# Kernel tuning notes

Hardware: AMD Instinct MI355X
Metric: run time of the kernel (lower is better)

Reference implementation:

```python
import jax, jax.numpy as jnp
import numpy as np

IMG_W, IMG_H = 704, 256
BN_EPS, LN_EPS = 1e-5, 1e-5


def _l2norm(x, axis):
    n = jnp.linalg.norm(x, axis=axis, keepdims=True)
    return x / jnp.maximum(n, 1e-12)


def _layernorm(x, g, b):
    m = jnp.mean(x, axis=-1, keepdims=True)
    v = jnp.var(x, axis=-1, keepdims=True)
    return (x - m) / jnp.sqrt(v + LN_EPS) * g + b


def _bilinear(ref, uv):
    # ref: (B, d, H, W); uv: (B, P, 2) pixel coords (x, y)
    B, d, H, W = ref.shape
    x, y = uv[..., 0], uv[..., 1]
    x0 = jnp.floor(x); y0 = jnp.floor(y)
    wx = x - x0; wy = y - y0
    valid = (x >= 0) & (x <= W - 1) & (y >= 0) & (y <= H - 1)
    x0i = jnp.clip(x0.astype(jnp.int32), 0, W - 1)
    x1i = jnp.clip(x0i + 1, 0, W - 1)
    y0i = jnp.clip(y0.astype(jnp.int32), 0, H - 1)
    y1i = jnp.clip(y0i + 1, 0, H - 1)
    ref_t = ref.reshape(B, d, H * W).transpose(0, 2, 1)  # (B, HW, d)
    g = lambda yy, xx: jnp.take_along_axis(ref_t, (yy * W + xx)[..., None], axis=1)
    val = (g(y0i, x0i) * ((1 - wx) * (1 - wy))[..., None]
           + g(y0i, x1i) * (wx * (1 - wy))[..., None]
           + g(y1i, x0i) * ((1 - wx) * wy)[..., None]
           + g(y1i, x1i) * (wx * wy)[..., None])  # (B, P, d)
    return val, valid.astype(ref.dtype)


def setup_inputs() -> dict:
    key = jax.random.key(0)
    ks = jax.random.split(key, 12)
    b, n, fd, dim, h, w = 2, 6, 128, 128, 64, 176
    feature = jax.random.normal(ks[0], (b, n, fd, h, w), jnp.float32)
    # intrinsics ~ [[500,0,352],[0,500,128],[0,0,1]]
    K = jnp.array([[500.0, 0.0, IMG_W / 2], [0.0, 500.0, IMG_H / 2], [0.0, 0.0, 1.0]], jnp.float32)
    I_src = jnp.broadcast_to(K, (b, n, 3, 3)).copy()
    I_tar_inv = jnp.broadcast_to(jnp.linalg.inv(K), (b, 3, 3)).copy()
    # extrinsics near identity: small rotation + small translation
    a = 0.02 * jax.random.normal(ks[1], (b, n, 3), jnp.float32)
    zeros = jnp.zeros((b, n), jnp.float32)
    skew = jnp.stack([
        jnp.stack([zeros, -a[..., 2], a[..., 1]], -1),
        jnp.stack([a[..., 2], zeros, -a[..., 0]], -1),
        jnp.stack([-a[..., 1], a[..., 0], zeros], -1)], -2)
    R = jnp.eye(3, dtype=jnp.float32) + skew
    T = 0.1 * jax.random.normal(ks[2], (b, n, 3, 1), jnp.float32)
    E = jnp.broadcast_to(jnp.eye(4, dtype=jnp.float32), (b, n, 4, 4)).copy()
    E = E.at[..., :3, :3].set(R).at[..., :3, 3:4].set(T)
    dis = 1.5 * jnp.ones((b, 1, 1, 1), jnp.float32)
    norm = jnp.array([0.0, 0.0, 1.0], jnp.float32)[None, None] + 0.01 * jax.random.normal(ks[3], (b, 1, 3), jnp.float32)
    s = 1.0 / np.sqrt(fd)
    return {
        'feature': feature, 'I_src': I_src, 'I_tar_inv': I_tar_inv, 'E': E, 'dis': dis, 'norm': norm,
        'conv_w': s * jax.random.normal(ks[4], (dim, fd), jnp.float32),
        'bn_gamma': jnp.ones((fd,), jnp.float32), 'bn_beta': jnp.zeros((fd,), jnp.float32),
        'bn_mean': 0.1 * jax.random.normal(ks[5], (fd,), jnp.float32),
        'bn_var': jax.random.uniform(ks[6], (fd,), jnp.float32, 0.5, 1.5),
        'ln1_g': jnp.ones((dim,), jnp.float32), 'ln1_b': jnp.zeros((dim,), jnp.float32),
        'ln2_g': jnp.ones((dim,), jnp.float32), 'ln2_b': jnp.zeros((dim,), jnp.float32),
        'mlp_w1': s * jax.random.normal(ks[7], (dim, 2 * dim), jnp.float32),
        'mlp_b1': jnp.zeros((2 * dim,), jnp.float32),
        'mlp_w2': (1.0 / np.sqrt(2 * fd)) * jax.random.normal(ks[8], (2 * dim, dim), jnp.float32),
        'mlp_b2': jnp.zeros((dim,), jnp.float32),
    }


def reference(feature, I_src, I_tar_inv, E, dis, norm, conv_w, bn_gamma, bn_beta, bn_mean, bn_var,
              ln1_g, ln1_b, ln2_g, ln2_b, mlp_w1, mlp_b1, mlp_w2, mlp_b2):
    b, n, fd, h, w = feature.shape
    dim = conv_w.shape[0]
    P = h * w
    # ---- pixel grid in [0,1], homogeneous ----
    xs = jnp.linspace(0.0, 1.0, w, dtype=feature.dtype)
    ys = jnp.linspace(0.0, 1.0, h, dtype=feature.dtype)
    X, Y = jnp.meshgrid(xs, ys)  # (h, w), x varies along width
    pix = jnp.stack([X, Y, jnp.ones_like(X)], 0).reshape(3, P)  # (3, P)
    img_wh1 = jnp.array([[IMG_W], [IMG_H], [1.0]], feature.dtype)  # (3,1)
    pix = pix * img_wh1
    # ---- homography H = I_src (R - T n^T / dis) I_tar_inv ----
    R = E[..., :3, :3]
    T = E[..., :3, 3:4]
    Hm = I_src @ (R - (T @ norm[:, None, :, :]) / dis) @ I_tar_inv[:, None, :, :]  # (b,n,3,3)
    homo = jnp.einsum('bnij,jp->bnip', Hm, pix)  # (b,n,3,P)
    homo = homo[:, :, :2] / homo[:, :, 2:]
    homo = homo / img_wh1[:2]  # back to 0..1
    uv = homo.transpose(0, 1, 3, 2).reshape(b * n, P, 2) * jnp.array([w, h], feature.dtype)
    # ---- feature_linear: BN(eval) -> ReLU -> 1x1 conv ----
    xf = (feature - bn_mean[:, None, None]) / jnp.sqrt(bn_var + BN_EPS)[:, None, None]
    xf = xf * bn_gamma[:, None, None] + bn_beta[:, None, None]
    xf = jax.nn.relu(xf)
    val = jnp.einsum('oc,bnchw->bnohw', conv_w, xf)  # (b,n,dim,h,w)
    query = val[:, 0]  # (b,dim,h,w)
    # ---- homography-guided bilinear sampling ----
    v, mask = _bilinear(val.reshape(b * n, dim, h, w), uv)  # (bn,P,dim), (bn,P)
    key_n = _l2norm(v, axis=2).reshape(b, n, P, dim)
    q = _l2norm(query.reshape(b, dim, P), axis=1)
    dot = jnp.einsum('bdp,bnpd->bnp', q, key_n)
    dot = dot * mask.reshape(b, n, P)
    att = jax.nn.softmax(dot, axis=1)
    z = jnp.einsum('bnp,bnpd->bpd', att, v.reshape(b, n, P, dim))
    z = z.transpose(0, 2, 1).reshape(b, dim, h, w)
    z = query + z
    # ---- MLP block ----
    z = z.reshape(b, dim, P).transpose(0, 2, 1)  # (b,P,dim)
    z = _layernorm(z, ln1_g, ln1_b)
    hdn = jax.nn.gelu(z @ mlp_w1 + mlp_b1, approximate=False)
    z = z + (hdn @ mlp_w2 + mlp_b2)
    z = _layernorm(z, ln2_g, ln2_b)
    return z.transpose(0, 2, 1).reshape(b, dim, h, w)
```

## Files before the change

### kernel.cpp

```cpp
#include <hip/hip_runtime.h>
#include <hip/hip_bf16.h>
#include <cstdint>
#include <cstddef>

#define B_   2
#define N_   6
#define FD_  128
#define DIM_ 128
#define H_   64
#define W_   176
#define P_   (H_*W_)
#define IMGW 704.0
#define IMGH 256.0
#define UVB  8

struct __align__(16) Samp { float wx, wy; int o00, o01; int o10, o11; int valid, pad; };

typedef __attribute__((ext_vector_type(8))) short short8;
typedef __attribute__((ext_vector_type(4))) float f32x4;

__device__ __forceinline__ float wave_sum(float v) {
#pragma unroll
  for (int off = 32; off > 0; off >>= 1) v += __shfl_xor(v, off, 64);
  return v;
}

__device__ __forceinline__ unsigned short f2bf(float f) {
  union { __hip_bfloat16 h; unsigned short u; } c;
  c.h = __float2bfloat16(f);
  return c.u;
}
__device__ __forceinline__ float bf2f(unsigned short s) {
  return __uint_as_float(((unsigned int)s) << 16);
}
__device__ __forceinline__ float bfx(uint2 u, int j) {
  unsigned int w = (j < 2) ? u.x : u.y;
  return bf2f((unsigned short)((j & 1) ? (w >> 16) : (w & 0xffffu)));
}

__global__ __launch_bounds__(256) void prep_kernel(const float* __restrict__ I_src, const float* __restrict__ I_tar_inv,
                           const float* __restrict__ E, const float* __restrict__ dis,
                           const float* __restrict__ nrm,
                           const float* __restrict__ bn_g, const float* __restrict__ bn_b,
                           const float* __restrict__ bn_m, const float* __restrict__ bn_v,
                           const float* __restrict__ w1, const float* __restrict__ w2,
                           const float* __restrict__ conv_w,
                           Samp* __restrict__ samp, float* __restrict__ bns, float* __restrict__ bnb,
                           short* __restrict__ w1b, short* __restrict__ w2b, short* __restrict__ cwb) {
  int blk = blockIdx.x;
  if (blk >= B_ * N_ * UVB) {
    int tid = (blk - B_ * N_ * UVB) * 256 + threadIdx.x;
    int f = tid >> 6, l = tid & 63;
    if (f < 64) {
      int nt = f >> 2, ks = f & 3;
      int n = nt * 16 + (l & 15);
      int kb = ks * 32 + (l >> 4) * 8;
#pragma unroll
      for (int j = 0; j < 8; ++j)
        w1b[((size_t)f * 64 + l) * 8 + j] = (short)f2bf(w1[(size_t)(kb + j) * 256 + n]);
    } else if (f < 128) {
      int g = f - 64;
      int nt = g >> 3, ks = g & 7;
      int n = nt * 16 + (l & 15);
      int kb = ks * 32 + (l >> 4) * 8;
#pragma unroll
      for (int j = 0; j < 8; ++j)
        w2b[((size_t)g * 64 + l) * 8 + j] = (short)f2bf(w2[(size_t)(kb + j) * 128 + n]);
    } else {
      int g2 = f - 128;
      int ot = g2 >> 2, ks = g2 & 3;
      int o  = ot * 16 + (l & 15);
      int cb = ks * 32 + (l >> 4) * 8;
#pragma unroll
      for (int j = 0; j < 8; ++j)
        cwb[((size_t)g2 * 64 + l) * 8 + j] = (short)f2bf(conv_w[(size_t)o * FD_ + cb + j]);
    }
    return;
  }
  int bn = blk / UVB;
  int part = blk % UVB;
  int bb = bn / N_;
  if (blk == 0 && threadIdx.x < FD_) {
    int t = threadIdx.x;
    float inv = 1.0f / sqrtf(bn_v[t] + 1e-5f);
    float sc = bn_g[t] * inv;
    bns[t] = sc;
    bnb[t] = bn_b[t] - bn_m[t] * sc;
  }
  const float* Ep = E + bn * 16;
  double R[9], T[3];
#pragma unroll
  for (int i = 0; i < 3; ++i) {
#pragma unroll
    for (int j = 0; j < 3; ++j) R[i*3+j] = (double)Ep[i*4+j];
    T[i] = (double)Ep[i*4+3];
  }
  double dd = (double)dis[bb];
  double M[9];
#pragma unroll
  for (int i = 0; i < 3; ++i)
#pragma unroll
    for (int j = 0; j < 3; ++j)
      M[i*3+j] = R[i*3+j] - T[i] * (double)nrm[bb*3+j] / dd;
  const float* Is = I_src + bn * 9;
  double A[9];
#pragma unroll
  for (int i = 0; i < 3; ++i)
#pragma unroll
    for (int j = 0; j < 3; ++j)
      A[i*3+j] = (double)Is[i*3+0]*M[0+j] + (double)Is[i*3+1]*M[3+j] + (double)Is[i*3+2]*M[6+j];
  const float* It = I_tar_inv + bb * 9;
  double Hm[9];
#pragma unroll
  for (int i = 0; i < 3; ++i)
#pragma unroll
    for (int j = 0; j < 3; ++j)
      Hm[i*3+j] = A[i*3+0]*(double)It[0+j] + A[i*3+1]*(double)It[3+j] + A[i*3+2]*(double)It[6+j];

  const double dx = 1.0 / (double)(W_ - 1);
  const double dy = 1.0 / (double)(H_ - 1);
  for (int p = part * 256 + threadIdx.x; p < P_; p += 256 * UVB) {
    int ii = p / W_;
    int jj = p - ii * W_;
    double xs = (jj == W_ - 1) ? 1.0 : (double)jj * dx;
    double ys = (ii == H_ - 1) ? 1.0 : (double)ii * dy;
    double px = xs * IMGW;
    double py = ys * IMGH;
    double hx = Hm[0]*px + Hm[1]*py + Hm[2];
    double hy = Hm[3]*px + Hm[4]*py + Hm[5];
    double hz = Hm[6]*px + Hm[7]*py + Hm[8];
    double u = ((hx / hz) / IMGW) * (double)W_;
    double v = ((hy / hz) / IMGH) * (double)H_;
    double x0 = floor(u), y0 = floor(v);
    bool valid = (u >= 0.0) && (u <= (double)(W_ - 1)) && (v >= 0.0) && (v <= (double)(H_ - 1));
    int x0i = min(max((int)x0, 0), W_ - 1);
    int x1i = min(x0i + 1, W_ - 1);
    int y0i = min(max((int)y0, 0), H_ - 1);
    int y1i = min(y0i + 1, H_ - 1);
    Samp s;
    s.wx = (float)(u - x0);
    s.wy = (float)(v - y0);
    s.o00 = (y0i * W_ + x0i) * DIM_;
    s.o01 = (y0i * W_ + x1i) * DIM_;
    s.o10 = (y1i * W_ + x0i) * DIM_;
    s.o11 = (y1i * W_ + x1i) * DIM_;
    s.valid = valid ? 1 : 0;
    s.pad = 0;
    samp[(size_t)bn * P_ + p] = s;
  }
}

__global__ __launch_bounds__(256) void conv_kernel(const float* __restrict__ feature,
    const short* __restrict__ cwb, const float* __restrict__ bns_g, const float* __restrict__ bnb_g,
    unsigned short* __restrict__ val_t) {
  __shared__ float bns_s[FD_], bnb_s[FD_];
  int t = threadIdx.x;
  if (t < FD_) { bns_s[t] = bns_g[t]; bnb_s[t] = bnb_g[t]; }
  __syncthreads();

  int bn = blockIdx.y;
  int p0 = blockIdx.x * 64;
  int lane = t & 63, wv = t >> 6;
  int m = lane & 15, quad = lane >> 4;
  int pw = wv * 16;

  const float* fb = feature + (size_t)bn * FD_ * P_ + p0 + pw + m;

  float xv[4][8];
#pragma unroll
  for (int ks = 0; ks < 4; ++ks)
#pragma unroll
    for (int j = 0; j < 8; ++j) {
      int c = ks * 32 + quad * 8 + j;
      xv[ks][j] = fb[(size_t)c * P_];
    }

  short8 Ah[4], Al[4];
#pragma unroll
  for (int ks = 0; ks < 4; ++ks)
#pragma unroll
    for (int j = 0; j < 8; ++j) {
      int c = ks * 32 + quad * 8 + j;
      float v = fmaxf(xv[ks][j] * bns_s[c] + bnb_s[c], 0.f);
      unsigned short h = f2bf(v);
      Ah[ks][j] = (short)h;
      Al[ks][j] = (short)f2bf(v - bf2f(h));
    }

  f32x4 acc[8];
#pragma unroll
  for (int ot = 0; ot < 8; ++ot) {
    f32x4 a = {0.f, 0.f, 0.f, 0.f};
#pragma unroll
    for (int ks = 0; ks < 4; ++ks) {
      short8 Bv = *(const short8*)(cwb + ((size_t)(ot * 4 + ks) * 64 + lane) * 8);
      a = __builtin_amdgcn_mfma_f32_16x16x32_bf16(Ah[ks], Bv, a, 0, 0, 0);
      a = __builtin_amdgcn_mfma_f32_16x16x32_bf16(Al[ks], Bv, a, 0, 0, 0);
    }
    acc[ot] = a;
  }

  unsigned short* vb = val_t + ((size_t)bn * P_ + p0 + pw + quad * 4) * DIM_ + m;
#pragma unroll
  for (int ot = 0; ot < 8; ++ot)
#pragma unroll
    for (int r = 0; r < 4; ++r)
      vb[(size_t)r * DIM_ + ot * 16] = f2bf(acc[ot][r]);
}

__global__ __launch_bounds__(256) void attn_kernel(const unsigned short* __restrict__ val_t,
    const Samp* __restrict__ samp,
    const float* __restrict__ ln1g, const float* __restrict__ ln1b,
    float* __restrict__ zln) {
  int lane = threadIdx.x & 63;
  int wv = threadIdx.x >> 6;
  int half = lane >> 5;
  int sl = lane & 31;
  int bid = blockIdx.x;
  int newbid = (bid & 7) * (gridDim.x >> 3) + (bid >> 3);
  int pt = newbid * 8 + wv * 2 + half;
  int bb = pt / P_;
  int p = pt - bb * P_;
  int d0 = sl << 2;

  uint2 uq = *(const uint2*)(val_t + ((size_t)(bb * N_) * P_ + p) * DIM_ + d0);
  float qv[4] = { bfx(uq, 0), bfx(uq, 1), bfx(uq, 2), bfx(uq, 3) };
  float qss = qv[0]*qv[0] + qv[1]*qv[1] + qv[2]*qv[2] + qv[3]*qv[3];
#pragma unroll
  for (int off = 1; off <= 16; off <<= 1) qss += __shfl_xor(qss, off, 64);
  float qinv = 1.0f / fmaxf(sqrtf(qss), 1e-12f);

  float dots[N_], vs[N_][4];
#pragma unroll
  for (int n = 0; n < N_; ++n) {
    Samp s = samp[(size_t)(bb * N_ + n) * P_ + p];
    const unsigned short* base = val_t + (size_t)(bb * N_ + n) * P_ * DIM_ + d0;
    uint2 u00 = *(const uint2*)(base + s.o00);
    uint2 u01 = *(const uint2*)(base + s.o01);
    uint2 u10 = *(const uint2*)(base + s.o10);
    uint2 u11 = *(const uint2*)(base + s.o11);
    float wx = s.wx, wy = s.wy;
    float w00 = (1.0f - wx) * (1.0f - wy), w01 = wx * (1.0f - wy);
    float w10 = (1.0f - wx) * wy,          w11 = wx * wy;
    float ss = 0.f, du = 0.f;
#pragma unroll
    for (int j = 0; j < 4; ++j) {
      float v = bfx(u00, j) * w00 + bfx(u01, j) * w01 + bfx(u10, j) * w10 + bfx(u11, j) * w11;
      vs[n][j] = v;
      ss += v * v;
      du += qv[j] * v;
    }
#pragma unroll
    for (int off = 1; off <= 16; off <<= 1) {
      ss += __shfl_xor(ss, off, 64);
      du += __shfl_xor(du, off, 64);
    }
    float kinv = 1.0f / fmaxf(sqrtf(ss), 1e-12f);
    dots[n] = s.valid ? (du * kinv * qinv) : 0.0f;
  }
  float mx = dots[0];
#pragma unroll
  for (int n = 1; n < N_; ++n) mx = fmaxf(mx, dots[n]);
  float es[N_], den = 0.f;
#pragma unroll
  for (int n = 0; n < N_; ++n) { es[n] = expf(dots[n] - mx); den += es[n]; }
  float dinv = 1.0f / den;
  float z[4] = { qv[0], qv[1], qv[2], qv[3] };
#pragma unroll
  for (int n = 0; n < N_; ++n) {
    float a = es[n] * dinv;
#pragma unroll
    for (int j = 0; j < 4; ++j) z[j] += a * vs[n][j];
  }
  float sz = z[0] + z[1] + z[2] + z[3];
  float q2 = z[0]*z[0] + z[1]*z[1] + z[2]*z[2] + z[3]*z[3];
#pragma unroll
  for (int off = 1; off <= 16; off <<= 1) {
    sz += __shfl_xor(sz, off, 64);
    q2 += __shfl_xor(q2, off, 64);
  }
  float mean = sz * (1.0f / DIM_);
  float var = fmaxf(q2 * (1.0f / DIM_) - mean * mean, 0.f);
  float rstd = rsqrtf(var + 1e-5f);
  float4 g4 = *(const float4*)(ln1g + d0);
  float4 b4 = *(const float4*)(ln1b + d0);
  float4 o4;
  o4.x = (z[0] - mean) * rstd * g4.x + b4.x;
  o4.y = (z[1] - mean) * rstd * g4.y + b4.y;
  o4.z = (z[2] - mean) * rstd * g4.z + b4.z;
  o4.w = (z[3] - mean) * rstd * g4.w + b4.w;
  *(float4*)(zln + (size_t)pt * DIM_ + d0) = o4;
}

__global__ __launch_bounds__(256) void mlp_kernel(const float* __restrict__ zln,
    const short* __restrict__ w1b, const short* __restrict__ w2b,
    const float* __restrict__ b1, const float* __restrict__ b2,
    const float* __restrict__ ln2g, const float* __restrict__ ln2b,
    float* __restrict__ out) {
  __shared__ __align__(16) char smem[17408];
  short* hh = (short*)smem;
  short* hl = (short*)(smem + 8448);
  float* pbuf = (float*)(smem + 16896);
  float* zo = (float*)smem;

  int t = threadIdx.x;
  int l = t & 63, ng = t >> 6;
  int m = l & 15, quad = l >> 4;
  int row0 = blockIdx.x * 16;

  const float* zr0 = zln + (size_t)(row0 + m) * DIM_;
  short8 A1h[4], A1l[4];
#pragma unroll
  for (int ks = 0; ks < 4; ++ks) {
    float4 xa = *(const float4*)(zr0 + ks * 32 + quad * 8);
    float4 xb = *(const float4*)(zr0 + ks * 32 + quad * 8 + 4);
    float v[8] = {xa.x, xa.y, xa.z, xa.w, xb.x, xb.y, xb.z, xb.w};
#pragma unroll
    for (int j = 0; j < 8; ++j) {
      unsigned short h = f2bf(v[j]);
      A1h[ks][j] = (short)h;
      A1l[ks][j] = (short)f2bf(v[j] - bf2f(h));
    }
  }

  float b1v[4];
#pragma unroll
  for (int i = 0; i < 4; ++i) b1v[i] = b1[(ng * 4 + i) * 16 + m];
  float res[2][4], b2v[2], g2v[2], be2v[2];
#pragma unroll
  for (int e = 0; e < 2; ++e) {
    int dt = ng * 2 + e;
    int d = dt * 16 + m;
    b2v[e] = b2[d]; g2v[e] = ln2g[d]; be2v[e] = ln2b[d];
#pragma unroll
    for (int r = 0; r < 4; ++r)
      res[e][r] = zln[(size_t)(row0 + quad * 4 + r) * DIM_ + dt * 16 + m];
  }

#pragma unroll
  for (int i = 0; i < 4; ++i) {
    int nt = ng * 4 + i;
    f32x4 a = {0.f, 0.f, 0.f, 0.f};
#pragma unroll
    for (int ks = 0; ks < 4; ++ks) {
      short8 Bv = *(const short8*)(w1b + ((size_t)(nt * 4 + ks) * 64 + l) * 8);
      a = __builtin_amdgcn_mfma_f32_16x16x32_bf16(A1h[ks], Bv, a, 0, 0, 0);
      a = __builtin_amdgcn_mfma_f32_16x16x32_bf16(A1l[ks], Bv, a, 0, 0, 0);
    }
#pragma unroll
    for (int r = 0; r < 4; ++r) {
      float hv = a[r] + b1v[i];
      float g = 0.5f * hv * (1.0f + erff(hv * 0.70710678118654752f));
      unsigned short gh = f2bf(g);
      int addr = (quad * 4 + r) * 264 + nt * 16 + m;
      hh[addr] = (short)gh;
      hl[addr] = (short)f2bf(g - bf2f(gh));
    }
  }
  __syncthreads();

  f32x4 acc2[2];
  acc2[0] = (f32x4){0.f, 0.f, 0.f, 0.f};
  acc2[1] = (f32x4){0.f, 0.f, 0.f, 0.f};
#pragma unroll
  for (int ks2 = 0; ks2 < 8; ++ks2) {
    short8 A2h = *(const short8*)&hh[m * 264 + ks2 * 32 + quad * 8];
    short8 A2l = *(const short8*)&hl[m * 264 + ks2 * 32 + quad * 8];
#pragma unroll
    for (int e = 0; e < 2; ++e) {
      int g = (ng * 2 + e) * 8 + ks2;
      short8 Bv = *(const short8*)(w2b + ((size_t)g * 64 + l) * 8);
      acc2[e] = __builtin_amdgcn_mfma_f32_16x16x32_bf16(A2h, Bv, acc2[e], 0, 0, 0);
      acc2[e] = __builtin_amdgcn_mfma_f32_16x16x32_bf16(A2l, Bv, acc2[e], 0, 0, 0);
    }
  }

  float z2[2][4];
#pragma unroll
  for (int e = 0; e < 2; ++e)
#pragma unroll
    for (int r = 0; r < 4; ++r)
      z2[e][r] = acc2[e][r] + b2v[e] + res[e][r];

  float ps[4], pq2[4];
#pragma unroll
  for (int r = 0; r < 4; ++r) {
    float s = z2[0][r] + z2[1][r];
    float q2 = z2[0][r]*z2[0][r] + z2[1][r]*z2[1][r];
#pragma unroll
    for (int off = 1; off <= 8; off <<= 1) {
      s  += __shfl_xor(s,  off, 64);
      q2 += __shfl_xor(q2, off, 64);
    }
    ps[r] = s; pq2[r] = q2;
  }
  if (m == 0) {
#pragma unroll
    for (int r = 0; r < 4; ++r) {
      pbuf[ng * 16 + quad * 4 + r]      = ps[r];
      pbuf[64 + ng * 16 + quad * 4 + r] = pq2[r];
    }
  }
  __syncthreads();

  float mean[4], rstd[4];
#pragma unroll
  for (int r = 0; r < 4; ++r) {
    int px = quad * 4 + r;
    float s = pbuf[px] + pbuf[16 + px] + pbuf[32 + px] + pbuf[48 + px];
    float q = pbuf[64 + px] + pbuf[80 + px] + pbuf[96 + px] + pbuf[112 + px];
    mean[r] = s * (1.0f / 128.0f);
    float var = fmaxf(q * (1.0f / 128.0f) - mean[r] * mean[r], 0.f);
    rstd[r] = rsqrtf(var + 1e-5f);
  }

#pragma unroll
  for (int e = 0; e < 2; ++e) {
    int dt = ng * 2 + e;
#pragma unroll
    for (int r = 0; r < 4; ++r) {
      float v = (z2[e][r] - mean[r]) * rstd[r] * g2v[e] + be2v[e];
      zo[(dt * 16 + m) * 20 + quad * 4 + r] = v;
    }
  }
  __syncthreads();

  int bb2 = row0 / P_;
  int p0 = row0 - bb2 * P_;
  float* ob = out + (size_t)bb2 * DIM_ * P_ + p0;
#pragma unroll
  for (int pass = 0; pass < 2; ++pass) {
    int idx = pass * 256 + t;
    int d = idx >> 2, fq = idx & 3;
    float4 v4 = *(float4*)&zo[d * 20 + fq * 4];
    *(float4*)(ob + (size_t)d * P_ + fq * 4) = v4;
  }
}

extern "C" void kernel_launch(void* const* d_in, const int* in_sizes, int n_in,
                              void* d_out, int out_size, void* d_ws, size_t ws_size,
                              hipStream_t stream) {
  const float* feature = (const float*)d_in[0];
  const float* I_src   = (const float*)d_in[1];
  const float* I_tar   = (const float*)d_in[2];
  const float* E       = (const float*)d_in[3];
  const float* dis     = (const float*)d_in[4];
  const float* nrm     = (const float*)d_in[5];
  const float* conv_w  = (const float*)d_in[6];
  const float* bn_g    = (const float*)d_in[7];
  const float* bn_b    = (const float*)d_in[8];
  const float* bn_m    = (const float*)d_in[9];
  const float* bn_v    = (const float*)d_in[10];
  const float* ln1g    = (const float*)d_in[11];
  const float* ln1b    = (const float*)d_in[12];
  const float* ln2g    = (const float*)d_in[13];
  const float* ln2b    = (const float*)d_in[14];
  const float* w1      = (const float*)d_in[15];
  const float* b1      = (const float*)d_in[16];
  const float* w2      = (const float*)d_in[17];
  const float* b2      = (const float*)d_in[18];
  float* out = (float*)d_out;

  float* wsf = (float*)d_ws;
  float* bns = wsf;
  float* bnb = wsf + 128;
  unsigned short* val_t = (unsigned short*)(wsf + 256);
  float* zln = (float*)(val_t + (size_t)B_ * N_ * P_ * DIM_);
  Samp*  samp = (Samp*)(zln + (size_t)B_ * P_ * DIM_);
  short* w1b = (short*)(samp + (size_t)B_ * N_ * P_);
  short* w2b = w1b + 32768;
  short* cwb = w2b + 32768;

  hipLaunchKernelGGL(prep_kernel, dim3(B_ * N_ * UVB + 40), dim3(256), 0, stream,
                     I_src, I_tar, E, dis, nrm, bn_g, bn_b, bn_m, bn_v, w1, w2, conv_w,
                     samp, bns, bnb, w1b, w2b, cwb);
  hipLaunchKernelGGL(conv_kernel, dim3(P_ / 64, B_ * N_), dim3(256), 0, stream,
                     feature, cwb, bns, bnb, val_t);
  hipLaunchKernelGGL(attn_kernel, dim3(B_ * P_ / 8), dim3(256), 0, stream,
                     val_t, samp, ln1g, ln1b, zln);
  hipLaunchKernelGGL(mlp_kernel, dim3(B_ * P_ / 16), dim3(256), 0, stream,
                     zln, w1b, w2b, b1, b2, ln2g, ln2b, out);
}
```

Measured before the change: 194.4 us.

## Fuse attention and MLP kernels, passing LayerNorm output through shared memory

Merges the attention/LN1 kernel and the MLP/LN2 kernel into one kernel that handles 16 pixels per block. The LN1 output goes to shared memory instead of a global fp32 buffer, which removes a global write and read of zln plus one launch. Each pixel now uses 16 lanes with 8-element (uint4) loads instead of 32 lanes with 4 elements, which widens gathers but raises per-thread register pressure. The cost is an extra block barrier, more shared memory per block, and possibly lower occupancy.

```diff
diff --git a/kernel.cpp b/kernel.cpp
--- a/kernel.cpp
+++ b/kernel.cpp
@@ -19,12 +19,6 @@
 typedef __attribute__((ext_vector_type(8))) short short8;
 typedef __attribute__((ext_vector_type(4))) float f32x4;
 
-__device__ __forceinline__ float wave_sum(float v) {
-#pragma unroll
-  for (int off = 32; off > 0; off >>= 1) v += __shfl_xor(v, off, 64);
-  return v;
-}
-
 __device__ __forceinline__ unsigned short f2bf(float f) {
   union { __hip_bfloat16 h; unsigned short u; } c;
   c.h = __float2bfloat16(f);
@@ -33,8 +27,8 @@
 __device__ __forceinline__ float bf2f(unsigned short s) {
   return __uint_as_float(((unsigned int)s) << 16);
 }
-__device__ __forceinline__ float bfx(uint2 u, int j) {
-  unsigned int w = (j < 2) ? u.x : u.y;
+__device__ __forceinline__ float bfx8(uint4 u, int j) {
+  unsigned int w = (j < 2) ? u.x : (j < 4) ? u.y : (j < 6) ? u.z : u.w;
   return bf2f((unsigned short)((j & 1) ? (w >> 16) : (w & 0xffffu)));
 }
 
@@ -208,50 +202,66 @@
       vb[(size_t)r * DIM_ + ot * 16] = f2bf(acc[ot][r]);
 }
 
-__global__ __launch_bounds__(256) void attn_kernel(const unsigned short* __restrict__ val_t,
+__global__ __launch_bounds__(256) void attn_mlp_kernel(const unsigned short* __restrict__ val_t,
     const Samp* __restrict__ samp,
     const float* __restrict__ ln1g, const float* __restrict__ ln1b,
-    float* __restrict__ zln) {
-  int lane = threadIdx.x & 63;
-  int wv = threadIdx.x >> 6;
-  int half = lane >> 5;
-  int sl = lane & 31;
+    const short* __restrict__ w1b, const short* __restrict__ w2b,
+    const float* __restrict__ b1, const float* __restrict__ b2,
+    const float* __restrict__ ln2g, const float* __restrict__ ln2b,
+    float* __restrict__ out) {
+  __shared__ __align__(16) char smem[25856];
+  float* zl   = (float*)smem;
+  short* hh   = (short*)(smem + 8448);
+  short* hl   = (short*)(smem + 16896);
+  float* pbuf = (float*)(smem + 25344);
+  float* zo   = (float*)smem;
+
+  int t = threadIdx.x;
+  int l = t & 63, wv = t >> 6;
+  int pq = l >> 4, sl = l & 15;
+  int m = l & 15, quad = l >> 4;
   int bid = blockIdx.x;
   int newbid = (bid & 7) * (gridDim.x >> 3) + (bid >> 3);
-  int pt = newbid * 8 + wv * 2 + half;
+  int row0 = newbid * 16;
+
+  int pt = row0 + wv * 4 + pq;
   int bb = pt / P_;
   int p = pt - bb * P_;
-  int d0 = sl << 2;
-
-  uint2 uq = *(const uint2*)(val_t + ((size_t)(bb * N_) * P_ + p) * DIM_ + d0);
-  float qv[4] = { bfx(uq, 0), bfx(uq, 1), bfx(uq, 2), bfx(uq, 3) };
-  float qss = qv[0]*qv[0] + qv[1]*qv[1] + qv[2]*qv[2] + qv[3]*qv[3];
-#pragma unroll
-  for (int off = 1; off <= 16; off <<= 1) qss += __shfl_xor(qss, off, 64);
+  int d0 = sl << 3;
+
+  uint4 uq = *(const uint4*)(val_t + ((size_t)(bb * N_) * P_ + p) * DIM_ + d0);
+  float qv[8];
+#pragma unroll
+  for (int j = 0; j < 8; ++j) qv[j] = bfx8(uq, j);
+  float qss = 0.f;
+#pragma unroll
+  for (int j = 0; j < 8; ++j) qss += qv[j] * qv[j];
+#pragma unroll
+  for (int off = 1; off <= 8; off <<= 1) qss += __shfl_xor(qss, off, 64);
   float qinv = 1.0f / fmaxf(sqrtf(qss), 1e-12f);
 
-  float dots[N_], vs[N_][4];
+  float dots[N_], vs[N_][8];
 #pragma unroll
   for (int n = 0; n < N_; ++n) {
     Samp s = samp[(size_t)(bb * N_ + n) * P_ + p];
     const unsigned short* base = val_t + (size_t)(bb * N_ + n) * P_ * DIM_ + d0;
-    uint2 u00 = *(const uint2*)(base + s.o00);
-    uint2 u01 = *(const uint2*)(base + s.o01);
-    uint2 u10 = *(const uint2*)(base + s.o10);
-    uint2 u11 = *(const uint2*)(base + s.o11);
+    uint4 u00 = *(const uint4*)(base + s.o00);
+    uint4 u01 = *(const uint4*)(base + s.o01);
+    uint4 u10 = *(const uint4*)(base + s.o10);
+    uint4 u11 = *(const uint4*)(base + s.o11);
     float wx = s.wx, wy = s.wy;
     float w00 = (1.0f - wx) * (1.0f - wy), w01 = wx * (1.0f - wy);
     float w10 = (1.0f - wx) * wy,          w11 = wx * wy;
     float ss = 0.f, du = 0.f;
 #pragma unroll
-    for (int j = 0; j < 4; ++j) {
-      float v = bfx(u00, j) * w00 + bfx(u01, j) * w01 + bfx(u10, j) * w10 + bfx(u11, j) * w11;
+    for (int j = 0; j < 8; ++j) {
+      float v = bfx8(u00, j) * w00 + bfx8(u01, j) * w01 + bfx8(u10, j) * w10 + bfx8(u11, j) * w11;
       vs[n][j] = v;
       ss += v * v;
       du += qv[j] * v;
     }
 #pragma unroll
-    for (int off = 1; off <= 16; off <<= 1) {
+    for (int off = 1; off <= 8; off <<= 1) {
       ss += __shfl_xor(ss, off, 64);
       du += __shfl_xor(du, off, 64);
     }
@@ -265,81 +275,74 @@
 #pragma unroll
   for (int n = 0; n < N_; ++n) { es[n] = expf(dots[n] - mx); den += es[n]; }
   float dinv = 1.0f / den;
-  float z[4] = { qv[0], qv[1], qv[2], qv[3] };
+  float z[8];
+#pragma unroll
+  for (int j = 0; j < 8; ++j) z[j] = qv[j];
 #pragma unroll
   for (int n = 0; n < N_; ++n) {
     float a = es[n] * dinv;
 #pragma unroll
-    for (int j = 0; j < 4; ++j) z[j] += a * vs[n][j];
-  }
-  float sz = z[0] + z[1] + z[2] + z[3];
-  float q2 = z[0]*z[0] + z[1]*z[1] + z[2]*z[2] + z[3]*z[3];
-#pragma unroll
-  for (int off = 1; off <= 16; off <<= 1) {
+    for (int j = 0; j < 8; ++j) z[j] += a * vs[n][j];
+  }
+  float sz = 0.f, q2 = 0.f;
+#pragma unroll
+  for (int j = 0; j < 8; ++j) { sz += z[j]; q2 += z[j] * z[j]; }
+#pragma unroll
+  for (int off = 1; off <= 8; off <<= 1) {
     sz += __shfl_xor(sz, off, 64);
     q2 += __shfl_xor(q2, off, 64);
   }
-  float mean = sz * (1.0f / DIM_);
-  float var = fmaxf(q2 * (1.0f / DIM_) - mean * mean, 0.f);
-  float rstd = rsqrtf(var + 1e-5f);
-  float4 g4 = *(const float4*)(ln1g + d0);
-  float4 b4 = *(const float4*)(ln1b + d0);
-  float4 o4;
-  o4.x = (z[0] - mean) * rstd * g4.x + b4.x;
-  o4.y = (z[1] - mean) * rstd * g4.y + b4.y;
-  o4.z = (z[2] - mean) * rstd * g4.z + b4.z;
-  o4.w = (z[3] - mean) * rstd * g4.w + b4.w;
-  *(float4*)(zln + (size_t)pt * DIM_ + d0) = o4;
-}
-
-__global__ __launch_bounds__(256) void mlp_kernel(const float* __restrict__ zln,
-    const short* __restrict__ w1b, const short* __restrict__ w2b,
-    const float* __restrict__ b1, const float* __restrict__ b2,
-    const float* __restrict__ ln2g, const float* __restrict__ ln2b,
-    float* __restrict__ out) {
-  __shared__ __align__(16) char smem[17408];
-  short* hh = (short*)smem;
-  short* hl = (short*)(smem + 8448);
-  float* pbuf = (float*)(smem + 16896);
-  float* zo = (float*)smem;
-
-  int t = threadIdx.x;
-  int l = t & 63, ng = t >> 6;
-  int m = l & 15, quad = l >> 4;
-  int row0 = blockIdx.x * 16;
-
-  const float* zr0 = zln + (size_t)(row0 + m) * DIM_;
-  short8 A1h[4], A1l[4];
-#pragma unroll
-  for (int ks = 0; ks < 4; ++ks) {
-    float4 xa = *(const float4*)(zr0 + ks * 32 + quad * 8);
-    float4 xb = *(const float4*)(zr0 + ks * 32 + quad * 8 + 4);
-    float v[8] = {xa.x, xa.y, xa.z, xa.w, xb.x, xb.y, xb.z, xb.w};
-#pragma unroll
-    for (int j = 0; j < 8; ++j) {
-      unsigned short h = f2bf(v[j]);
-      A1h[ks][j] = (short)h;
-      A1l[ks][j] = (short)f2bf(v[j] - bf2f(h));
-    }
-  }
+  float mean1 = sz * (1.0f / DIM_);
+  float var1 = fmaxf(q2 * (1.0f / DIM_) - mean1 * mean1, 0.f);
+  float rstd1 = rsqrtf(var1 + 1e-5f);
+  float4 ga = *(const float4*)(ln1g + d0);
+  float4 gb = *(const float4*)(ln1g + d0 + 4);
+  float4 ba = *(const float4*)(ln1b + d0);
+  float4 bbv = *(const float4*)(ln1b + d0 + 4);
+  float4 oa, ob4;
+  oa.x  = (z[0] - mean1) * rstd1 * ga.x + ba.x;
+  oa.y  = (z[1] - mean1) * rstd1 * ga.y + ba.y;
+  oa.z  = (z[2] - mean1) * rstd1 * ga.z + ba.z;
+  oa.w  = (z[3] - mean1) * rstd1 * ga.w + ba.w;
+  ob4.x = (z[4] - mean1) * rstd1 * gb.x + bbv.x;
+  ob4.y = (z[5] - mean1) * rstd1 * gb.y + bbv.y;
+  ob4.z = (z[6] - mean1) * rstd1 * gb.z + bbv.z;
+  ob4.w = (z[7] - mean1) * rstd1 * gb.w + bbv.w;
+  float* zrow = &zl[(wv * 4 + pq) * 132 + d0];
+  *(float4*)zrow = oa;
+  *(float4*)(zrow + 4) = ob4;
+  __syncthreads();
 
   float b1v[4];
 #pragma unroll
-  for (int i = 0; i < 4; ++i) b1v[i] = b1[(ng * 4 + i) * 16 + m];
+  for (int i = 0; i < 4; ++i) b1v[i] = b1[(wv * 4 + i) * 16 + m];
   float res[2][4], b2v[2], g2v[2], be2v[2];
 #pragma unroll
   for (int e = 0; e < 2; ++e) {
-    int dt = ng * 2 + e;
+    int dt = wv * 2 + e;
     int d = dt * 16 + m;
     b2v[e] = b2[d]; g2v[e] = ln2g[d]; be2v[e] = ln2b[d];
 #pragma unroll
     for (int r = 0; r < 4; ++r)
-      res[e][r] = zln[(size_t)(row0 + quad * 4 + r) * DIM_ + dt * 16 + m];
+      res[e][r] = zl[(quad * 4 + r) * 132 + dt * 16 + m];
+  }
+
+  short8 A1h[4], A1l[4];
+  const float* zr0 = &zl[m * 132];
+#pragma unroll
+  for (int ks = 0; ks < 4; ++ks) {
+#pragma unroll
+    for (int j = 0; j < 8; ++j) {
+      float v = zr0[ks * 32 + quad * 8 + j];
+      unsigned short h = f2bf(v);
+      A1h[ks][j] = (short)h;
+      A1l[ks][j] = (short)f2bf(v - bf2f(h));
+    }
   }
 
 #pragma unroll
   for (int i = 0; i < 4; ++i) {
-    int nt = ng * 4 + i;
+    int nt = wv * 4 + i;
     f32x4 a = {0.f, 0.f, 0.f, 0.f};
 #pragma unroll
     for (int ks = 0; ks < 4; ++ks) {
@@ -368,7 +371,7 @@
     short8 A2l = *(const short8*)&hl[m * 264 + ks2 * 32 + quad * 8];
 #pragma unroll
     for (int e = 0; e < 2; ++e) {
-      int g = (ng * 2 + e) * 8 + ks2;
+      int g = (wv * 2 + e) * 8 + ks2;
       short8 Bv = *(const short8*)(w2b + ((size_t)g * 64 + l) * 8);
       acc2[e] = __builtin_amdgcn_mfma_f32_16x16x32_bf16(A2h, Bv, acc2[e], 0, 0, 0);
       acc2[e] = __builtin_amdgcn_mfma_f32_16x16x32_bf16(A2l, Bv, acc2[e], 0, 0, 0);
@@ -386,19 +389,19 @@
 #pragma unroll
   for (int r = 0; r < 4; ++r) {
     float s = z2[0][r] + z2[1][r];
-    float q2 = z2[0][r]*z2[0][r] + z2[1][r]*z2[1][r];
+    float q = z2[0][r]*z2[0][r] + z2[1][r]*z2[1][r];
 #pragma unroll
     for (int off = 1; off <= 8; off <<= 1) {
-      s  += __shfl_xor(s,  off, 64);
-      q2 += __shfl_xor(q2, off, 64);
-    }
-    ps[r] = s; pq2[r] = q2;
+      s += __shfl_xor(s, off, 64);
+      q += __shfl_xor(q, off, 64);
+    }
+    ps[r] = s; pq2[r] = q;
   }
   if (m == 0) {
 #pragma unroll
     for (int r = 0; r < 4; ++r) {
-      pbuf[ng * 16 + quad * 4 + r]      = ps[r];
-      pbuf[64 + ng * 16 + quad * 4 + r] = pq2[r];
+      pbuf[wv * 16 + quad * 4 + r]      = ps[r];
+      pbuf[64 + wv * 16 + quad * 4 + r] = pq2[r];
     }
   }
   __syncthreads();
@@ -416,7 +419,7 @@
 
 #pragma unroll
   for (int e = 0; e < 2; ++e) {
-    int dt = ng * 2 + e;
+    int dt = wv * 2 + e;
 #pragma unroll
     for (int r = 0; r < 4; ++r) {
       float v = (z2[e][r] - mean[r]) * rstd[r] * g2v[e] + be2v[e];
@@ -476,8 +479,6 @@
                      samp, bns, bnb, w1b, w2b, cwb);
   hipLaunchKernelGGL(conv_kernel, dim3(P_ / 64, B_ * N_), dim3(256), 0, stream,
                      feature, cwb, bns, bnb, val_t);
-  hipLaunchKernelGGL(attn_kernel, dim3(B_ * P_ / 8), dim3(256), 0, stream,
-                     val_t, samp, ln1g, ln1b, zln);
-  hipLaunchKernelGGL(mlp_kernel, dim3(B_ * P_ / 16), dim3(256), 0, stream,
-                     zln, w1b, w2b, b1, b2, ln2g, ln2b, out);
-}
+  hipLaunchKernelGGL(attn_mlp_kernel, dim3(B_ * P_ / 16), dim3(256), 0, stream,
+                     val_t, samp, ln1g, ln1b, w1b, w2b, b1, b2, ln2g, ln2b, out);
+}
```

Result: faster. 181.3 us (-6.8%).
